# Kernel optimization log

Measured on AMD Instinct MI355X. Metric: run time of the kernel, lower is better.

## Reference

```python
import jax, jax.numpy as jnp
import numpy as np

DECAY = 0.99
EPSILON = 1e-05
CODEBOOK_SIZE = 1024
DIM = 128


def setup_inputs() -> dict:
    key = jax.random.key(0)
    k1, k2, k3, k4 = jax.random.split(key, 4)
    x = jax.random.normal(k1, (8, 8192, DIM), dtype=jnp.float32)
    embed = jax.random.normal(k2, (CODEBOOK_SIZE, DIM), dtype=jnp.float32)
    cluster_size = jax.random.uniform(k3, (CODEBOOK_SIZE,), dtype=jnp.float32)
    embed_avg = jax.random.normal(k4, (CODEBOOK_SIZE, DIM), dtype=jnp.float32)
    return {"x": x, "embed": embed, "cluster_size": cluster_size, "embed_avg": embed_avg}


def reference(x, embed, cluster_size, embed_avg):
    shape = x.shape
    flat = x.reshape(-1, shape[-1])  # [N, dim]

    # quantize: negative squared euclidean distance, argmax == nearest code
    dist = -(jnp.sum(flat * flat, axis=1, keepdims=True)
             - 2.0 * flat @ embed.T
             + jnp.sum(embed * embed, axis=1)[None, :])  # [N, K]
    embed_ind = jnp.argmax(dist, axis=-1)  # [N]

    quantize = embed[embed_ind].reshape(shape)            # dequantize
    embed_ind_out = embed_ind.reshape(shape[:-1])

    # training-time EMA updates (one-hot expressed as segment_sum)
    batch_cluster_size = jax.ops.segment_sum(
        jnp.ones_like(embed_ind, dtype=flat.dtype), embed_ind,
        num_segments=CODEBOOK_SIZE)                       # == one_hot.sum(0)
    new_cluster_size = cluster_size * DECAY + (1.0 - DECAY) * batch_cluster_size

    embed_sum = jax.ops.segment_sum(flat, embed_ind,
                                    num_segments=CODEBOOK_SIZE)  # == (x.T @ one_hot).T
    new_embed_avg = embed_avg * DECAY + (1.0 - DECAY) * embed_sum

    total = new_cluster_size.sum()
    smoothed = (new_cluster_size + EPSILON) / (total + CODEBOOK_SIZE * EPSILON)
    smoothed_counts = smoothed * total
    new_embed = new_embed_avg / smoothed_counts[:, None]

    return quantize, embed_ind_out, new_cluster_size, new_embed_avg, new_embed
```

## Files before the change

kernel.cpp:

```cpp
#include <hip/hip_runtime.h>
#include <math.h>

#define DIM 128
#define KCODES 1024
#define NROWS 65536

typedef short bf16x8 __attribute__((ext_vector_type(8)));
typedef float f32x4 __attribute__((ext_vector_type(4)));

#define WS_COUNTS 0
#define WS_ESUM   1024
#define WS_IOFF   132096
#define WS_TOTAL  133120
#define WS_ENORM2 133124
#define WS_EBF    134148
#define WS_WIN    461828
#define WS_SORTED 527364
#define WS_SCODE  592900

#define OFF_Q   0
#define OFF_IND 8388608
#define OFF_NCS 8454144
#define OFF_NEA 8455168
#define OFF_NE  8586240


static __device__ __forceinline__ unsigned short f2bf(float f) {
    unsigned u = __float_as_uint(f);
    unsigned r = (u + 0x7FFFu + ((u >> 16) & 1u)) >> 16;
    return (unsigned short)r;
}

static __device__ __forceinline__ void gload_lds16(const unsigned short* g,
                                                   unsigned short* l) {
    __builtin_amdgcn_global_load_lds(
        (const __attribute__((address_space(1))) void*)g,
        (__attribute__((address_space(3))) void*)l, 16, 0, 0);
}

__global__ __launch_bounds__(64) void k_prep(const float* __restrict__ embed,
                                             unsigned short* __restrict__ ebf,
                                             float* __restrict__ en2,
                                             float* __restrict__ counts,
                                             float* __restrict__ esum,
                                             int* __restrict__ cursor) {
    int k = blockIdx.x;
    int l = threadIdx.x;
    if (l == 0) { counts[k] = 0.0f; cursor[k] = 0; }
    *(float2*)&esum[(size_t)k * DIM + l * 2] = (float2){0.0f, 0.0f};
    float2 v = *(const float2*)&embed[(size_t)k * DIM + l * 2];
    ushort2 b;
    b.x = f2bf(v.x);
    b.y = f2bf(v.y);
    *(ushort2*)&ebf[(k * DIM + l * 2) ^ ((k & 7) << 3)] = b;
    float s = v.x * v.x + v.y * v.y;
    #pragma unroll
    for (int off = 32; off; off >>= 1) s += __shfl_xor(s, off);
    if (l == 0) en2[k] = 512.0f - 0.5f * s;
}

__global__ __launch_bounds__(512, 4) void k_fused(const float* __restrict__ x,
                                                  const float* __restrict__ embed,
                                                  const unsigned short* __restrict__ ebf,
                                                  const float* __restrict__ en2g,
                                                  int* __restrict__ win_g,
                                                  float* __restrict__ counts,
                                                  float* __restrict__ out) {
    __shared__ unsigned short buf[2][128 * 128];
    __shared__ float en2s[KCODES];
    __shared__ int winS[128];

    const int tid = threadIdx.x;
    const int row0 = blockIdx.x * 128;

    #pragma unroll
    for (int i = 0; i < 2; ++i) en2s[i * 512 + tid] = en2g[i * 512 + tid];

    #pragma unroll
    for (int i = 0; i < 8; ++i) {
        int idx4 = i * 512 + tid;
        int lin = idx4 * 4;
        int r = lin >> 7, d = lin & 127;
        float4 v = *(const float4*)&x[(size_t)(row0 + r) * DIM + d];
        ushort4 b;
        b.x = f2bf(v.x); b.y = f2bf(v.y); b.z = f2bf(v.z); b.w = f2bf(v.w);
        *(ushort4*)&buf[0][(r * 128 + d) ^ ((r & 7) << 3)] = b;
    }
    __syncthreads();

    const int lane = tid & 63;
    const int wv = tid >> 6;
    const int ch = wv & 1;
    const int rh = (wv >> 1) * 32;
    const int l15 = lane & 15;
    const int q = lane >> 4;
    const int swz = (l15 & 7) << 3;

    #pragma unroll
    for (int i = 0; i < 4; ++i) {
        int idx8 = i * 512 + tid;
        gload_lds16(&ebf[idx8 * 8], &buf[1][idx8 * 8]);
    }

    bf16x8 af[4][2];
    #pragma unroll
    for (int ks = 0; ks < 4; ++ks)
        #pragma unroll
        for (int t = 0; t < 2; ++t)
            af[ks][t] = *(const bf16x8*)&buf[0][((rh + t * 16 + l15) * 128 + ks * 32 + q * 8) ^ swz];
    __syncthreads();

    float m1[2][4], m2[2][4];
    #pragma unroll
    for (int a = 0; a < 2; ++a)
        #pragma unroll
        for (int b = 0; b < 4; ++b) { m1[a][b] = 0.0f; m2[a][b] = 0.0f; }

    for (int ct = 0; ct < 8; ++ct) {
        const int c0 = ct * 128;
        const unsigned short* cbuf = buf[1 ^ (ct & 1)];

        if (ct < 7) {
            unsigned short* nbuf = buf[ct & 1];
            const unsigned short* gsrc = ebf + (size_t)(c0 + 128) * DIM;
            #pragma unroll
            for (int i = 0; i < 4; ++i) {
                int idx8 = i * 512 + tid;
                gload_lds16(&gsrc[idx8 * 8], &nbuf[idx8 * 8]);
            }
        }

        f32x4 acc[2][4];
        #pragma unroll
        for (int cl = 0; cl < 4; ++cl) {
            float en = en2s[c0 + ch * 64 + cl * 16 + l15];
            #pragma unroll
            for (int rt = 0; rt < 2; ++rt) acc[rt][cl] = (f32x4){en, en, en, en};
        }

        __builtin_amdgcn_s_setprio(1);
        #pragma unroll
        for (int ks = 0; ks < 4; ++ks) {
            bf16x8 bfr[4];
            #pragma unroll
            for (int cl = 0; cl < 4; ++cl)
                bfr[cl] = *(const bf16x8*)&cbuf[((ch * 64 + cl * 16 + l15) * 128 + ks * 32 + q * 8) ^ swz];
            #pragma unroll
            for (int rt = 0; rt < 2; ++rt)
                #pragma unroll
                for (int cl = 0; cl < 4; ++cl)
                    acc[rt][cl] = __builtin_amdgcn_mfma_f32_16x16x32_bf16(af[ks][rt], bfr[cl],
                                                                          acc[rt][cl], 0, 0, 0);
        }

        #pragma unroll
        for (int cp = 0; cp < 2; ++cp) {
            unsigned cu0 = (unsigned)(c0 + ch * 64 + cp * 32 + l15);
            unsigned cu1 = cu0 + 16u;
            #pragma unroll
            for (int rt = 0; rt < 2; ++rt)
                #pragma unroll
                for (int rg = 0; rg < 4; ++rg) {
                    float sa = acc[rt][cp * 2][rg];
                    float sb = acc[rt][cp * 2 + 1][rg];
                    float a = __uint_as_float((__float_as_uint(sa) & ~1023u) | cu0);
                    float b = __uint_as_float((__float_as_uint(sb) & ~1023u) | cu1);
                    m2[rt][rg] = fmaxf(m2[rt][rg],
                                       __builtin_amdgcn_fmed3f(a, b, m1[rt][rg]));
                    m1[rt][rg] = fmaxf(fmaxf(a, b), m1[rt][rg]);
                }
        }
        __builtin_amdgcn_s_setprio(0);

        __syncthreads();
    }

    float* scratch = (float*)buf[0];
    unsigned* hist = (unsigned*)buf[0] + 512;

    #pragma unroll
    for (int rt = 0; rt < 2; ++rt)
        #pragma unroll
        for (int rg = 0; rg < 4; ++rg) {
            float a1 = m1[rt][rg], a2 = m2[rt][rg];
            #pragma unroll
            for (int off = 1; off <= 8; off <<= 1) {
                float o1 = __shfl_xor(a1, off);
                float o2 = __shfl_xor(a2, off);
                float t = fmaxf(a2, o2);
                a2 = __builtin_amdgcn_fmed3f(a1, o1, t);
                a1 = fmaxf(a1, o1);
            }
            if (l15 == 0) {
                int row = rh + rt * 16 + q * 4 + rg;
                scratch[row * 4 + ch * 2 + 0] = a1;
                scratch[row * 4 + ch * 2 + 1] = a2;
            }
        }

    #pragma unroll
    for (int i = 0; i < 2; ++i) hist[i * 512 + tid] = 0u;
    __syncthreads();

    {
        const int sub = tid & 15;
        const int g = tid >> 4;
        #pragma unroll 2
        for (int rr = 0; rr < 4; ++rr) {
            const int lrow = g * 4 + rr;
            const float* sp = &scratch[lrow * 4];
            int ci[4];
            ci[0] = (int)(__float_as_uint(sp[0]) & 1023u);
            ci[1] = (int)(__float_as_uint(sp[1]) & 1023u);
            ci[2] = (int)(__float_as_uint(sp[2]) & 1023u);
            ci[3] = (int)(__float_as_uint(sp[3]) & 1023u);

            const float* xr = &x[(size_t)(row0 + lrow) * DIM + sub * 4];
            float4 xa = *(const float4*)xr;
            float4 xb = *(const float4*)(xr + 64);

            float d[4];
            #pragma unroll
            for (int j = 0; j < 4; ++j) {
                const float* er2 = &embed[(size_t)ci[j] * DIM + sub * 4];
                float4 ea4 = *(const float4*)er2;
                float4 eb4 = *(const float4*)(er2 + 64);
                float t0 = xa.x - ea4.x;
                float t1 = xa.y - ea4.y;
                float t2 = xa.z - ea4.z;
                float t3 = xa.w - ea4.w;
                float t4 = xb.x - eb4.x;
                float t5 = xb.y - eb4.y;
                float t6 = xb.z - eb4.z;
                float t7 = xb.w - eb4.w;
                d[j] = ((t0 * t0 + t1 * t1) + (t2 * t2 + t3 * t3)) +
                       ((t4 * t4 + t5 * t5) + (t6 * t6 + t7 * t7));
            }
            #pragma unroll
            for (int off = 1; off <= 8; off <<= 1) {
                #pragma unroll
                for (int j = 0; j < 4; ++j) d[j] += __shfl_xor(d[j], off);
            }

            int win = ci[0];
            float dw = d[0];
            #pragma unroll
            for (int j = 1; j < 4; ++j) {
                bool b = (d[j] < dw) || (d[j] == dw && ci[j] < win);
                dw = b ? d[j] : dw;
                win = b ? ci[j] : win;
            }
            if (sub == 0) winS[lrow] = win;
        }
    }
    __syncthreads();

    if (tid < 128) {
        int w = winS[tid];
        atomicAdd(&hist[w], 1u);
        win_g[row0 + tid] = w;
        out[OFF_IND + row0 + tid] = (float)w;
    }

    #pragma unroll 4
    for (int i = 0; i < 16; ++i) {
        int lrow = wv * 16 + i;
        int w = winS[lrow];
        float2 v = *(const float2*)&embed[(size_t)w * DIM + lane * 2];
        *(float2*)&out[OFF_Q + (size_t)(row0 + lrow) * DIM + lane * 2] = v;
    }

    __syncthreads();
    #pragma unroll
    for (int i = 0; i < 2; ++i) {
        unsigned c = hist[i * 512 + tid];
        if (c) atomicAdd(&counts[i * 512 + tid], (float)c);
    }
}

__global__ __launch_bounds__(1024) void k_scansort(const float* __restrict__ cs,
                                                   const int* __restrict__ win_arr,
                                                   float* __restrict__ ws,
                                                   int* __restrict__ sorted,
                                                   int* __restrict__ scode,
                                                   float* __restrict__ out) {
    __shared__ int h[KCODES];
    __shared__ int bs[KCODES];
    __shared__ int wsum[16];
    __shared__ float wtot[16];
    const float* counts = ws + WS_COUNTS;
    int* cursor = (int*)(ws + WS_IOFF);

    const int t = threadIdx.x;
    h[t] = 0;
    __syncthreads();
    const int row = blockIdx.x * 1024 + t;
    const int w = win_arr[row];
    const int r = atomicAdd(&h[w], 1);

    const int lane = t & 63, wvi = t >> 6;
    const float cf = counts[t];
    const int c = (int)cf;
    int v = c;
    #pragma unroll
    for (int off = 1; off < 64; off <<= 1) {
        int o = __shfl_up(v, off);
        if (lane >= off) v += o;
    }
    if (lane == 63) wsum[wvi] = v;
    if (blockIdx.x == 0) {
        float ncs = cs[t] * 0.99f + 0.01f * cf;
        out[OFF_NCS + t] = ncs;
        float nf = ncs;
        #pragma unroll
        for (int off = 32; off; off >>= 1) nf += __shfl_xor(nf, off);
        if (lane == 0) wtot[wvi] = nf;
    }
    __syncthreads();

    int base = 0;
    for (int i = 0; i < wvi; ++i) base += wsum[i];
    const int gbase = base + v - c;

    if (blockIdx.x == 0 && t == 0) {
        float tt = 0.f;
        for (int i = 0; i < 16; ++i) tt += wtot[i];
        ws[WS_TOTAL] = tt;
    }

    const int cnt = h[t];
    if (cnt) bs[t] = gbase + atomicAdd(&cursor[t], cnt);
    __syncthreads();
    const int pos = bs[w] + r;
    sorted[pos] = row;
    scode[pos] = w;
}

__global__ __launch_bounds__(256) void k_segsum(const float* __restrict__ x,
                                                const int* __restrict__ sorted,
                                                const int* __restrict__ scode,
                                                float* __restrict__ esum) {
    const int lane = threadIdx.x & 63;
    const int wv = threadIdx.x >> 6;
    const int base = blockIdx.x * 256 + wv * 64;
    const int l15 = lane & 15;

    float ax = 0.f, ay = 0.f;
    int cur = -1;

    #pragma unroll
    for (int cc = 0; cc < 4; ++cc) {
        const int p = base + cc * 16 + l15;
        const int srow = sorted[p];
        const int sc = scode[p];
        if (cc == 0) cur = __shfl(sc, 0);
        #pragma unroll
        for (int j = 0; j < 16; ++j) {
            int row = __shfl(srow, j);
            int c = __shfl(sc, j);
            if (c != cur) {
                atomicAdd(&esum[cur * DIM + lane * 2], ax);
                atomicAdd(&esum[cur * DIM + lane * 2 + 1], ay);
                ax = 0.f; ay = 0.f;
                cur = c;
            }
            float2 v = *(const float2*)&x[(size_t)row * DIM + lane * 2];
            ax += v.x;
            ay += v.y;
        }
    }
    atomicAdd(&esum[cur * DIM + lane * 2], ax);
    atomicAdd(&esum[cur * DIM + lane * 2 + 1], ay);
}

__global__ __launch_bounds__(256) void k_embed(const float* __restrict__ ea,
                                               const float* __restrict__ ws,
                                               float* __restrict__ out) {
    int i = blockIdx.x * 256 + threadIdx.x;
    int k = i >> 7;
    float nea = ea[i] * 0.99f + 0.01f * ws[WS_ESUM + i];
    out[OFF_NEA + i] = nea;
    float total = ws[WS_TOTAL];
    float ncs = out[OFF_NCS + k];
    float sm = (ncs + 1e-5f) / (total + 1024.0f * 1e-5f);
    out[OFF_NE + i] = nea / (sm * total);
}

extern "C" void kernel_launch(void* const* d_in, const int* in_sizes, int n_in,
                              void* d_out, int out_size, void* d_ws, size_t ws_size,
                              hipStream_t stream) {
    const float* x     = (const float*)d_in[0];
    const float* embed = (const float*)d_in[1];
    const float* cs    = (const float*)d_in[2];
    const float* ea    = (const float*)d_in[3];
    float* out = (float*)d_out;
    float* ws  = (float*)d_ws;

    k_prep<<<KCODES, 64, 0, stream>>>(embed, (unsigned short*)(ws + WS_EBF),
                                      ws + WS_ENORM2, ws + WS_COUNTS, ws + WS_ESUM,
                                      (int*)(ws + WS_IOFF));
    k_fused<<<NROWS / 128, 512, 0, stream>>>(x, embed,
                                             (const unsigned short*)(ws + WS_EBF),
                                             ws + WS_ENORM2, (int*)(ws + WS_WIN),
                                             ws + WS_COUNTS, out);
    k_scansort<<<NROWS / 1024, 1024, 0, stream>>>(cs, (const int*)(ws + WS_WIN), ws,
                                                  (int*)(ws + WS_SORTED),
                                                  (int*)(ws + WS_SCODE), out);
    k_segsum<<<NROWS / 256, 256, 0, stream>>>(x, (const int*)(ws + WS_SORTED),
                                              (const int*)(ws + WS_SCODE), ws + WS_ESUM);
    k_embed<<<131072 / 256, 256, 0, stream>>>(ea, ws, out);
}
```

Measured before the change: 151.7 us.

## Use 4-stage 64-code LDS ring with fine-grained vmcnt waits for codebook streaming

Replaces the 2-buffer 128-code double buffering of the bf16 codebook with a 4-slot ring of 64-code tiles, prefetching three tiles ahead. Each iteration waits only on the oldest outstanding async loads (vmcnt) before a barrier, instead of a full __syncthreads. The goal is to keep more global-to-LDS traffic in flight and hide load latency behind MFMA work. The cost is more loop iterations and barriers, each with half the MFMA work, plus reliance on exact vmcnt counting for correctness.

```diff
diff --git a/kernel.cpp b/kernel.cpp
--- a/kernel.cpp
+++ b/kernel.cpp
@@ -66,7 +66,7 @@
                                                   int* __restrict__ win_g,
                                                   float* __restrict__ counts,
                                                   float* __restrict__ out) {
-    __shared__ unsigned short buf[2][128 * 128];
+    __shared__ unsigned short buf[32768];
     __shared__ float en2s[KCODES];
     __shared__ int winS[128];
 
@@ -84,7 +84,7 @@
         float4 v = *(const float4*)&x[(size_t)(row0 + r) * DIM + d];
         ushort4 b;
         b.x = f2bf(v.x); b.y = f2bf(v.y); b.z = f2bf(v.z); b.w = f2bf(v.w);
-        *(ushort4*)&buf[0][(r * 128 + d) ^ ((r & 7) << 3)] = b;
+        *(ushort4*)&buf[(r * 128 + d) ^ ((r & 7) << 3)] = b;
     }
     __syncthreads();
 
@@ -96,19 +96,24 @@
     const int q = lane >> 4;
     const int swz = (l15 & 7) << 3;
 
-    #pragma unroll
-    for (int i = 0; i < 4; ++i) {
-        int idx8 = i * 512 + tid;
-        gload_lds16(&ebf[idx8 * 8], &buf[1][idx8 * 8]);
-    }
-
     bf16x8 af[4][2];
     #pragma unroll
     for (int ks = 0; ks < 4; ++ks)
         #pragma unroll
         for (int t = 0; t < 2; ++t)
-            af[ks][t] = *(const bf16x8*)&buf[0][((rh + t * 16 + l15) * 128 + ks * 32 + q * 8) ^ swz];
-    __syncthreads();
+            af[ks][t] = *(const bf16x8*)&buf[((rh + t * 16 + l15) * 128 + ks * 32 + q * 8) ^ swz];
+    __syncthreads();
+
+    #pragma unroll
+    for (int t = 0; t < 3; ++t) {
+        #pragma unroll
+        for (int i = 0; i < 2; ++i) {
+            int idx8 = i * 512 + tid;
+            gload_lds16(&ebf[t * 8192 + idx8 * 8], &buf[t * 8192 + idx8 * 8]);
+        }
+    }
+    asm volatile("s_waitcnt vmcnt(4)" ::: "memory");
+    __builtin_amdgcn_s_barrier();
 
     float m1[2][4], m2[2][4];
     #pragma unroll
@@ -116,24 +121,25 @@
         #pragma unroll
         for (int b = 0; b < 4; ++b) { m1[a][b] = 0.0f; m2[a][b] = 0.0f; }
 
-    for (int ct = 0; ct < 8; ++ct) {
-        const int c0 = ct * 128;
-        const unsigned short* cbuf = buf[1 ^ (ct & 1)];
-
-        if (ct < 7) {
-            unsigned short* nbuf = buf[ct & 1];
-            const unsigned short* gsrc = ebf + (size_t)(c0 + 128) * DIM;
-            #pragma unroll
-            for (int i = 0; i < 4; ++i) {
+    for (int ct = 0; ct < 16; ++ct) {
+        const int c0 = ct * 64;
+        const unsigned short* cbuf = &buf[(ct & 3) * 8192];
+
+        if (ct <= 12) {
+            const int tn = ct + 3;
+            unsigned short* nbuf = &buf[(tn & 3) * 8192];
+            const unsigned short* gsrc = &ebf[tn * 8192];
+            #pragma unroll
+            for (int i = 0; i < 2; ++i) {
                 int idx8 = i * 512 + tid;
                 gload_lds16(&gsrc[idx8 * 8], &nbuf[idx8 * 8]);
             }
         }
 
-        f32x4 acc[2][4];
-        #pragma unroll
-        for (int cl = 0; cl < 4; ++cl) {
-            float en = en2s[c0 + ch * 64 + cl * 16 + l15];
+        f32x4 acc[2][2];
+        #pragma unroll
+        for (int cl = 0; cl < 2; ++cl) {
+            float en = en2s[c0 + ch * 32 + cl * 16 + l15];
             #pragma unroll
             for (int rt = 0; rt < 2; ++rt) acc[rt][cl] = (f32x4){en, en, en, en};
         }
@@ -141,28 +147,27 @@
         __builtin_amdgcn_s_setprio(1);
         #pragma unroll
         for (int ks = 0; ks < 4; ++ks) {
-            bf16x8 bfr[4];
-            #pragma unroll
-            for (int cl = 0; cl < 4; ++cl)
-                bfr[cl] = *(const bf16x8*)&cbuf[((ch * 64 + cl * 16 + l15) * 128 + ks * 32 + q * 8) ^ swz];
+            bf16x8 bfr[2];
+            #pragma unroll
+            for (int cl = 0; cl < 2; ++cl)
+                bfr[cl] = *(const bf16x8*)&cbuf[((ch * 32 + cl * 16 + l15) * 128 + ks * 32 + q * 8) ^ swz];
             #pragma unroll
             for (int rt = 0; rt < 2; ++rt)
                 #pragma unroll
-                for (int cl = 0; cl < 4; ++cl)
+                for (int cl = 0; cl < 2; ++cl)
                     acc[rt][cl] = __builtin_amdgcn_mfma_f32_16x16x32_bf16(af[ks][rt], bfr[cl],
                                                                           acc[rt][cl], 0, 0, 0);
         }
 
-        #pragma unroll
-        for (int cp = 0; cp < 2; ++cp) {
-            unsigned cu0 = (unsigned)(c0 + ch * 64 + cp * 32 + l15);
+        {
+            unsigned cu0 = (unsigned)(c0 + ch * 32 + l15);
             unsigned cu1 = cu0 + 16u;
             #pragma unroll
             for (int rt = 0; rt < 2; ++rt)
                 #pragma unroll
                 for (int rg = 0; rg < 4; ++rg) {
-                    float sa = acc[rt][cp * 2][rg];
-                    float sb = acc[rt][cp * 2 + 1][rg];
+                    float sa = acc[rt][0][rg];
+                    float sb = acc[rt][1][rg];
                     float a = __uint_as_float((__float_as_uint(sa) & ~1023u) | cu0);
                     float b = __uint_as_float((__float_as_uint(sb) & ~1023u) | cu1);
                     m2[rt][rg] = fmaxf(m2[rt][rg],
@@ -172,11 +177,20 @@
         }
         __builtin_amdgcn_s_setprio(0);
 
-        __syncthreads();
-    }
-
-    float* scratch = (float*)buf[0];
-    unsigned* hist = (unsigned*)buf[0] + 512;
+        if (ct < 15) {
+            if (ct < 13) {
+                asm volatile("s_waitcnt vmcnt(4)" ::: "memory");
+            } else if (ct == 13) {
+                asm volatile("s_waitcnt vmcnt(2)" ::: "memory");
+            } else {
+                asm volatile("s_waitcnt vmcnt(0)" ::: "memory");
+            }
+            __builtin_amdgcn_s_barrier();
+        }
+    }
+
+    float* scratch = (float*)buf;
+    unsigned* hist = (unsigned*)buf + 512;
 
     #pragma unroll
     for (int rt = 0; rt < 2; ++rt)
```

After: 151.1 us. Within noise of the previous version (-0.4%).
